# Kernel optimization log

Hardware: AMD Instinct MI355X
Metric: run time of the kernel (lower is better)

Reference implementation:

```python
import jax, jax.numpy as jnp
import numpy as np

B, N, DIM = 2, 2048, 1024
HEADS, DIM_HEAD = 16, 64
SOFTCAP = 50.0
ROPE_THETA = 10000.0


def setup_inputs() -> dict:
    key = jax.random.key(0)
    k1, k2, k3 = jax.random.split(key, 3)
    x = jax.random.normal(k1, (B, N, DIM), jnp.float32)
    # structured modality positions: (type, offset, length), non-overlapping, in-bounds
    mods = np.zeros((B, 4, 3), np.int64)
    base_offsets = [200, 700, 1200, 1700]
    for b in range(B):
        for m, o in enumerate(base_offsets):
            mods[b, m] = (0, o + b * 16, 256)
    modalities = jnp.asarray(mods)
    gamma = jnp.zeros((DIM,), jnp.float32)           # RMSNorm gamma (init zeros, used as gamma+1)
    w_qkv = jax.random.normal(k2, (DIM, 3 * HEADS * DIM_HEAD), jnp.float32) * 0.02
    w_out = jax.random.normal(k3, (HEADS * DIM_HEAD, DIM), jnp.float32) * 0.02
    return {"x": x, "modalities": modalities, "gamma": gamma, "w_qkv": w_qkv, "w_out": w_out}


def _rotate_half(x):
    # interleaved-pair rotation, matching rotary-embedding-torch default
    x1, x2 = x[..., 0::2], x[..., 1::2]
    return jnp.stack((-x2, x1), axis=-1).reshape(x.shape)


def reference(x, modalities, gamma, w_qkv, w_out):
    b, n, d = x.shape
    h, dh = HEADS, DIM_HEAD
    seq = jnp.arange(n)
    off = modalities[..., 1]      # [b, m]
    length = modalities[..., 2]   # [b, m]

    # --- modality-aware rotary positions (span interior shrunk by offset [1, -1]) ---
    in_span = (seq[None, None, :] >= (off + 1)[:, :, None]) & (seq[None, None, :] < (off + length)[:, :, None])
    is_any_modality = in_span.any(axis=1)                                   # [b, n]
    pos = (seq[None, :] - jnp.cumsum(is_any_modality.astype(jnp.int32), axis=-1)).astype(jnp.float32)

    # --- RMSNorm: l2norm(x) * sqrt(d) * (gamma + 1) ---
    norm = jnp.maximum(jnp.sqrt(jnp.sum(x * x, axis=-1, keepdims=True)), 1e-12)
    xn = x / norm * jnp.sqrt(jnp.float32(d)) * (gamma + 1.0)

    # --- qkv projection, split heads -> [b, h, n, dh] ---
    qkv = (xn @ w_qkv).reshape(b, n, 3, h, dh)
    q, k, v = jnp.moveaxis(qkv, 2, 0)        # each [b, n, h, dh]
    q = jnp.transpose(q, (0, 2, 1, 3))
    k = jnp.transpose(k, (0, 2, 1, 3))
    v = jnp.transpose(v, (0, 2, 1, 3))

    # --- rotary embedding with modality-aware positions ---
    inv_freq = ROPE_THETA ** (-jnp.arange(0, dh, 2, dtype=jnp.float32) / dh)  # [dh/2]
    ang = pos[:, None, :, None] * inv_freq                                    # [b, 1, n, dh/2]
    ang = jnp.repeat(ang, 2, axis=-1)                                         # [b, 1, n, dh]
    cos, sin = jnp.cos(ang), jnp.sin(ang)
    q = q * cos + _rotate_half(q) * sin
    k = k * cos + _rotate_half(k) * sin

    # --- transfusion attention mask: causal OR per-modality bidirectional span ---
    causal_mask = seq[:, None] >= seq[None, :]                                 # [n, n]
    q_ge = seq[None, None, :] >= off[:, :, None]                               # [b, m, n]
    kv_lt = seq[None, None, :] < (off + length)[:, :, None]                    # [b, m, n]
    mod_mask = (q_ge[:, :, :, None] & kv_lt[:, :, None, :]).any(axis=1)        # [b, n, n]
    mask = causal_mask[None] | mod_mask                                        # [b, n, n]

    # --- attention with softclamp(50) ---
    scale = dh ** -0.5
    sim = jnp.einsum('bhid,bhjd->bhij', q, k) * scale
    sim = jnp.tanh(sim / SOFTCAP) * SOFTCAP
    sim = jnp.where(mask[:, None], sim, jnp.finfo(sim.dtype).min)
    attn = jax.nn.softmax(sim, axis=-1)
    out = jnp.einsum('bhij,bhjd->bhid', attn, v)                               # [b, h, n, dh]
    out = jnp.transpose(out, (0, 2, 1, 3)).reshape(b, n, h * dh)
    return out @ w_out
```

## Files before the change

### kernel.cpp

```cpp
#include <hip/hip_runtime.h>
#include <hip/hip_bf16.h>
#include <stdint.h>

#define B_ 2
#define N_ 2048
#define H_ 16
#define DIM_ 1024
#define NH3 3072
#define ROWS (B_*N_)
#define BHN (B_*H_*N_)

typedef __attribute__((ext_vector_type(8))) short bf16x8;
typedef __attribute__((ext_vector_type(4))) float f32x4;
typedef unsigned short u16;

__device__ __forceinline__ u16 f2bf(float f){
  union { float f; uint32_t u; } v; v.f = f;
  return (u16)((v.u + 0x7fffu + ((v.u >> 16) & 1u)) >> 16);
}

#if __has_builtin(__builtin_amdgcn_exp2f)
#define EXP2F(x) __builtin_amdgcn_exp2f(x)
#else
#define EXP2F(x) __expf((x) * 0.6931471805599453f)
#endif
#if __has_builtin(__builtin_amdgcn_rcpf)
#define RCPF(x) __builtin_amdgcn_rcpf(x)
#else
#define RCPF(x) (1.0f / (x))
#endif

#define GLL16(g, l) __builtin_amdgcn_global_load_lds( \
    (const __attribute__((address_space(1))) void*)(g), \
    (__attribute__((address_space(3))) void*)(l), 16, 0, 0)

__global__ __launch_bounds__(256) void k_prep(
    const float* __restrict__ x, const float* __restrict__ gamma,
    const float* __restrict__ wqkv, const float* __restrict__ wout,
    const int* __restrict__ mods,
    u16* __restrict__ xn, u16* __restrict__ wqkvT, u16* __restrict__ woutT,
    float* __restrict__ cosT, float* __restrict__ sinT)
{
  __shared__ float tile[32][33];
  const int bx = blockIdx.x;
  const int tid = threadIdx.x;
  if (bx < 4096){
    const int row = bx;
    const float4 xv = ((const float4*)(x + (size_t)row*DIM_))[tid];
    float ss = xv.x*xv.x + xv.y*xv.y + xv.z*xv.z + xv.w*xv.w;
#pragma unroll
    for (int d = 1; d < 64; d <<= 1) ss += __shfl_xor(ss, d);
    if ((tid & 63) == 0) tile[1][tid >> 6] = ss;
    __syncthreads();
    float tot = tile[1][0] + tile[1][1] + tile[1][2] + tile[1][3];
    float scl = 32.0f / fmaxf(sqrtf(tot), 1e-12f);
    const float4 gv = ((const float4*)gamma)[tid];
    ushort4 o;
    o.x = f2bf(xv.x * scl * (gv.x + 1.0f));
    o.y = f2bf(xv.y * scl * (gv.y + 1.0f));
    o.z = f2bf(xv.z * scl * (gv.z + 1.0f));
    o.w = f2bf(xv.w * scl * (gv.w + 1.0f));
    ((ushort4*)(xn + (size_t)row*DIM_))[tid] = o;
  } else if (bx < 8192){
    const int t = bx - 4096;
    const int bxx = t & 127, by = t >> 7;
    const float* src; u16* dst; int C, bc;
    if (bxx < 96){ src = wqkv; dst = wqkvT; C = NH3;  bc = bxx*32; }
    else         { src = wout; dst = woutT; C = DIM_; bc = (bxx-96)*32; }
    const int R = DIM_;
    const int tx = tid & 31, ty = tid >> 5;
    const int br = by * 32;
#pragma unroll
    for (int i = 0; i < 32; i += 8)
      tile[ty + i][tx] = src[(size_t)(br + ty + i)*C + bc + tx];
    __syncthreads();
#pragma unroll
    for (int i = 0; i < 32; i += 8)
      dst[(size_t)(bc + ty + i)*R + br + tx] = f2bf(tile[tx][ty + i]);
  } else {
    const int t = (bx - 8192)*256 + tid;
    const int f = t & 31, bn = t >> 5;
    const int b = bn >> 11, n = bn & (N_-1);
    int cum = 0;
#pragma unroll
    for (int m = 0; m < 4; ++m){
      const int off = mods[(b*4 + m)*3 + 1];
      const int len = mods[(b*4 + m)*3 + 2];
      cum += min(max(n - off, 0), len - 1);
    }
    const float pos = (float)(n - cum);
    const float inv = powf(10000.0f, -(float)(2*f) / 64.0f);
    float s, c;
    sincosf(pos * inv, &s, &c);
    cosT[t] = c; sinT[t] = s;
  }
}

template<int MODE, int BM>
__global__ __launch_bounds__(256) void k_gemm(
    const u16* __restrict__ A, const u16* __restrict__ Bt,
    int K, int Nc,
    float* __restrict__ outf,
    const float* __restrict__ cosT, const float* __restrict__ sinT,
    u16* __restrict__ qo, u16* __restrict__ ko, u16* __restrict__ vt)
{
  constexpr int MR = BM/32;
  constexpr int RA = BM/8;
  constexpr int CNT = (RA + 16)/4;
  __shared__ u16 lA[BM*64];
  __shared__ u16 lB[128*64];
  const int tid = threadIdx.x;
  const int wid = tid >> 6, lane = tid & 63;
  const int nx = gridDim.x;
  const int orig = blockIdx.y * nx + blockIdx.x;
  const int qq = (nx * gridDim.y) >> 3;
  const int wgid = (orig & 7) * qq + (orig >> 3);
  const int m0 = (wgid % nx) * BM, n0 = (wgid / nx) * 128;
  const int wm = wid >> 1, wn = wid & 1;
  const int srow = lane >> 3, sch = lane & 7;
  const int r16 = lane & 15, g4 = lane >> 4;
  f32x4 acc[MR][4] = {};
  const int ksteps = K >> 6;
  for (int kt = 0; kt < ksteps; ++kt){
    const int kb = kt*64;
    const int gch = sch ^ srow;
#pragma unroll
    for (int i = 0; i < CNT; ++i){
      const int reg = wid*CNT + i;
      if (reg < RA){
        const int row = reg*8 + srow;
        GLL16(A + (size_t)(m0 + row)*K + kb + gch*8, &lA[reg*512]);
      } else {
        const int r2 = reg - RA;
        const int row = r2*8 + srow;
        GLL16(Bt + (size_t)(n0 + row)*K + kb + gch*8, &lB[r2*512]);
      }
    }
    __syncthreads();
#pragma unroll
    for (int t = 0; t < 2; ++t){
      bf16x8 af[MR], bfr[4];
#pragma unroll
      for (int m = 0; m < MR; ++m){
        int row = wm*(BM/2) + m*16 + r16;
        int ch = (t*4 + g4) ^ (r16 & 7);
        af[m] = *(const bf16x8*)&lA[row*64 + ch*8];
      }
#pragma unroll
      for (int n = 0; n < 4; ++n){
        int row = wn*64 + n*16 + r16;
        int ch = (t*4 + g4) ^ (r16 & 7);
        bfr[n] = *(const bf16x8*)&lB[row*64 + ch*8];
      }
#pragma unroll
      for (int m = 0; m < MR; ++m)
#pragma unroll
        for (int n = 0; n < 4; ++n)
          acc[m][n] = __builtin_amdgcn_mfma_f32_16x16x32_bf16(af[m], bfr[n], acc[m][n], 0, 0, 0);
    }
    __syncthreads();
  }
#pragma unroll
  for (int m = 0; m < MR; ++m){
#pragma unroll
    for (int n = 0; n < 4; ++n){
      if constexpr (MODE == 0){
        const int gcol = n0 + wn*64 + n*16 + r16;
        const int s3 = gcol >> 10, hh = (gcol >> 6) & 15, d = gcol & 63;
        const int grow0 = m0 + wm*(BM/2) + m*16 + g4*4;
        const int b = grow0 >> 11, nn0 = grow0 & (N_-1);
        const size_t hb = (size_t)(b*H_ + hh);
        if (s3 == 2){
          uint32_t w01, w23;
          asm("v_cvt_pk_bf16_f32 %0, %1, %2" : "=v"(w01) : "v"(acc[m][n][0]), "v"(acc[m][n][1]));
          asm("v_cvt_pk_bf16_f32 %0, %1, %2" : "=v"(w23) : "v"(acc[m][n][2]), "v"(acc[m][n][3]));
          *reinterpret_cast<uint2*>(&vt[(hb*64 + d)*N_ + nn0]) = make_uint2(w01, w23);
        } else {
#pragma unroll
          for (int r = 0; r < 4; ++r){
            const float v = acc[m][n][r];
            const float part = __shfl_xor(v, 1);
            const int nn = nn0 + r;
            const int pidx = (b*N_ + nn)*32 + (d >> 1);
            const float c = cosT[pidx], sn = sinT[pidx];
            const float rot = (d & 1) ? (v*c + part*sn) : (v*c - part*sn);
            const u16 val = f2bf(rot);
            if (s3 == 0) qo[(hb*N_ + nn)*64 + d] = val;
            else         ko[(hb*N_ + nn)*64 + d] = val;
          }
        }
      } else {
#pragma unroll
        for (int r = 0; r < 4; ++r){
          const int grow = m0 + wm*(BM/2) + m*16 + g4*4 + r;
          const int gcol = n0 + wn*64 + n*16 + r16;
          outf[(size_t)grow*Nc + gcol] = acc[m][n][r];
        }
      }
    }
  }
}

#define PST 68
__global__ __launch_bounds__(256) void k_attn(
    const u16* __restrict__ qb, const u16* __restrict__ kb, const u16* __restrict__ vt,
    const int* __restrict__ mods, u16* __restrict__ xo)
{
  __shared__ u16 lK[64*64];
  __shared__ u16 lV[64*64];
  __shared__ u16 lP[4*16*PST];
  const int tid = threadIdx.x, wid = tid >> 6, lane = tid & 63;
  const int id = blockIdx.x;
  const int xcd = id & 7, rank = id >> 3;
  const int bh = xcd + 8*(rank & 3);
  const int qt = 31 - (rank >> 2);
  const int b = bh >> 4, h = bh & 15;
  const int r16 = lane & 15, g4 = lane >> 4;
  const int srow = lane >> 3, sch = lane & 7;
  int moff[4], mend[4];
#pragma unroll
  for (int m = 0; m < 4; ++m){
    moff[m] = mods[(b*4+m)*3+1];
    mend[m] = moff[m] + mods[(b*4+m)*3+2];
  }
  const u16* kbase = kb + (size_t)bh*N_*64;
  const u16* vbase = vt + (size_t)bh*64*N_;
  u16* lPw = &lP[wid*16*PST];

  const int q0 = qt*64 + wid*16;
  const int i  = q0 + r16;
  const int imax = qt*64 + 63;
  int jmax = 0;
#pragma unroll
  for (int m = 0; m < 4; ++m)
    if (i >= moff[m]) jmax = max(jmax, mend[m]);
  const u16* qrow = qb + ((size_t)bh*N_ + q0 + r16)*64;
  const bf16x8 aq0 = *(const bf16x8*)&qrow[g4*8];
  const bf16x8 aq1 = *(const bf16x8*)&qrow[32 + g4*8];
  f32x4 o[4] = {};
  f32x4 acc_s = {};
  bf16x8 ones;
#pragma unroll
  for (int j = 0; j < 8; ++j) ones[j] = (short)0x3F80;

  const float D1 = 0.18033688011112043f;
  const float D3 = -3.7570183356483704e-07f;

  for (int kt = 0; kt < N_/64; ++kt){
    bool proc = (kt*64 <= imax);
    if (!proc){
#pragma unroll
      for (int m = 0; m < 4; ++m)
        if (imax >= moff[m] && kt*64 < mend[m]) proc = true;
    }
    if (!proc) continue;
    __syncthreads();
#pragma unroll
    for (int ld = 0; ld < 2; ++ld){
      int reg = wid*2 + ld;
      int row = reg*8 + srow;
      int gch = sch ^ srow;
      GLL16(kbase + (size_t)(kt*64 + row)*64 + gch*8, &lK[reg*512]);
      GLL16(vbase + (size_t)row*N_ + kt*64 + gch*8,   &lV[reg*512]);
    }
    __syncthreads();
    f32x4 s[4] = {};
    __builtin_amdgcn_s_setprio(1);
#pragma unroll
    for (int cb = 0; cb < 4; ++cb){
#pragma unroll
      for (int t = 0; t < 2; ++t){
        int row = cb*16 + r16;
        int ch = (t*4 + g4) ^ (row & 7);
        bf16x8 bk = *(const bf16x8*)&lK[row*64 + ch*8];
        s[cb] = __builtin_amdgcn_mfma_f32_16x16x32_bf16(bk, t ? aq1 : aq0, s[cb], 0, 0, 0);
      }
    }
    __builtin_amdgcn_s_setprio(0);
    const int thr = max(i, jmax - 1) - kt*64;
    const bool nomask = (kt*64 + 63 <= q0);
#pragma unroll
    for (int cb = 0; cb < 4; ++cb){
      float p[4];
#pragma unroll
      for (int r = 0; r < 4; ++r){
        const float sv = s[cb][r];
        const float w = sv*sv;
        p[r] = EXP2F(sv * fmaf(w, D3, D1));
      }
      if (!nomask){
#pragma unroll
        for (int r = 0; r < 4; ++r)
          p[r] = (cb*16 + g4*4 + r <= thr) ? p[r] : 0.0f;
      }
      uint32_t w01, w23;
      asm("v_cvt_pk_bf16_f32 %0, %1, %2" : "=v"(w01) : "v"(p[0]), "v"(p[1]));
      asm("v_cvt_pk_bf16_f32 %0, %1, %2" : "=v"(w23) : "v"(p[2]), "v"(p[3]));
      *reinterpret_cast<uint2*>(&lPw[r16*PST + cb*16 + g4*4]) = make_uint2(w01, w23);
    }
    asm volatile("s_waitcnt lgkmcnt(0)" ::: "memory");
    __builtin_amdgcn_sched_barrier(0);
    union { uint2 h[2]; bf16x8 v; } u0, u1;
    u0.h[0] = *(const uint2*)&lPw[r16*PST + g4*8];
    u0.h[1] = *(const uint2*)&lPw[r16*PST + g4*8 + 4];
    u1.h[0] = *(const uint2*)&lPw[r16*PST + 32 + g4*8];
    u1.h[1] = *(const uint2*)&lPw[r16*PST + 32 + g4*8 + 4];
    __builtin_amdgcn_s_setprio(1);
    acc_s = __builtin_amdgcn_mfma_f32_16x16x32_bf16(u0.v, ones, acc_s, 0, 0, 0);
    acc_s = __builtin_amdgcn_mfma_f32_16x16x32_bf16(u1.v, ones, acc_s, 0, 0, 0);
#pragma unroll
    for (int cb = 0; cb < 4; ++cb){
#pragma unroll
      for (int t = 0; t < 2; ++t){
        int d = cb*16 + r16;
        int ch = (t*4 + g4) ^ (d & 7);
        bf16x8 bv = *(const bf16x8*)&lV[d*64 + ch*8];
        o[cb] = __builtin_amdgcn_mfma_f32_16x16x32_bf16(t ? u1.v : u0.v, bv, o[cb], 0, 0, 0);
      }
    }
    __builtin_amdgcn_s_setprio(0);
  }
#pragma unroll
  for (int r = 0; r < 4; ++r){
    const float linv = RCPF(acc_s[r]);
    const int iq = q0 + g4*4 + r;
#pragma unroll
    for (int cb = 0; cb < 4; ++cb)
      xo[(size_t)(b*N_ + iq)*DIM_ + h*64 + cb*16 + r16] = f2bf(o[cb][r]*linv);
  }
}

extern "C" void kernel_launch(void* const* d_in, const int* in_sizes, int n_in,
                              void* d_out, int out_size, void* d_ws, size_t ws_size,
                              hipStream_t stream){
  const float* x     = (const float*)d_in[0];
  const int*   mods  = (const int*)d_in[1];
  const float* gamma = (const float*)d_in[2];
  const float* wqkv  = (const float*)d_in[3];
  const float* wout  = (const float*)d_in[4];
  float* outp = (float*)d_out;

  char* p = (char*)d_ws;
  auto alloc = [&](size_t bytes) -> char* {
    char* r = p; p += (bytes + 255) & ~(size_t)255; return r;
  };
  float* cosT  = (float*)alloc((size_t)B_*N_*32*4);
  float* sinT  = (float*)alloc((size_t)B_*N_*32*4);
  u16* wqkvT   = (u16*)alloc((size_t)NH3*DIM_*2);
  u16* woutT   = (u16*)alloc((size_t)DIM_*DIM_*2);
  u16* xn      = (u16*)alloc((size_t)ROWS*DIM_*2);
  u16* qbb     = (u16*)alloc((size_t)BHN*64*2);
  u16* kbb     = (u16*)alloc((size_t)BHN*64*2);
  u16* vtb     = (u16*)alloc((size_t)BHN*64*2);
  u16* xo      = (u16*)alloc((size_t)ROWS*DIM_*2);

  k_prep<<<8704, 256, 0, stream>>>(x, gamma, wqkv, wout, mods, xn, wqkvT, woutT, cosT, sinT);
  k_gemm<0,128><<<dim3(ROWS/128, NH3/128), 256, 0, stream>>>(xn, wqkvT, DIM_, NH3, nullptr, cosT, sinT, qbb, kbb, vtb);
  k_attn<<<1024, 256, 0, stream>>>(qbb, kbb, vtb, mods, xo);
  k_gemm<1,64><<<dim3(ROWS/64, DIM_/128), 256, 0, stream>>>(xo, woutT, DIM_, DIM_, outp, nullptr, nullptr, nullptr, nullptr, nullptr);
}
```

Before: 117.0 us.

## Process 128-key tiles per barrier pair with swizzled P layout and hoisted load addresses

Result: no change. 116.9 us (-0.2%).

```diff
diff --git a/kernel.cpp b/kernel.cpp
--- a/kernel.cpp
+++ b/kernel.cpp
@@ -201,14 +201,13 @@
   }
 }
 
-#define PST 68
 __global__ __launch_bounds__(256) void k_attn(
     const u16* __restrict__ qb, const u16* __restrict__ kb, const u16* __restrict__ vt,
     const int* __restrict__ mods, u16* __restrict__ xo)
 {
-  __shared__ u16 lK[64*64];
-  __shared__ u16 lV[64*64];
-  __shared__ u16 lP[4*16*PST];
+  __shared__ u16 lK[128*64];
+  __shared__ u16 lV[64*128];
+  __shared__ u16 lP[4*16*64];
   const int tid = threadIdx.x, wid = tid >> 6, lane = tid & 63;
   const int id = blockIdx.x;
   const int xcd = id & 7, rank = id >> 3;
@@ -216,7 +215,6 @@
   const int qt = 31 - (rank >> 2);
   const int b = bh >> 4, h = bh & 15;
   const int r16 = lane & 15, g4 = lane >> 4;
-  const int srow = lane >> 3, sch = lane & 7;
   int moff[4], mend[4];
 #pragma unroll
   for (int m = 0; m < 4; ++m){
@@ -225,7 +223,7 @@
   }
   const u16* kbase = kb + (size_t)bh*N_*64;
   const u16* vbase = vt + (size_t)bh*64*N_;
-  u16* lPw = &lP[wid*16*PST];
+  u16* lPw = &lP[wid*16*64];
 
   const int q0 = qt*64 + wid*16;
   const int i  = q0 + r16;
@@ -234,6 +232,7 @@
 #pragma unroll
   for (int m = 0; m < 4; ++m)
     if (i >= moff[m]) jmax = max(jmax, mend[m]);
+  const int thrbase = max(i, jmax - 1);
   const u16* qrow = qb + ((size_t)bh*N_ + q0 + r16)*64;
   const bf16x8 aq0 = *(const bf16x8*)&qrow[g4*8];
   const bf16x8 aq1 = *(const bf16x8*)&qrow[32 + g4*8];
@@ -243,82 +242,114 @@
 #pragma unroll
   for (int j = 0; j < 8; ++j) ones[j] = (short)0x3F80;
 
+  const int srow8 = lane >> 3, sch8 = lane & 7;
+  const int srow4 = lane >> 4, sch16 = lane & 15;
+  const u16* kSrc0; const u16* kSrc1; const u16* kSrc2; const u16* kSrc3;
+  const u16* vSrc0; const u16* vSrc1; const u16* vSrc2; const u16* vSrc3;
+  {
+    const int kch = sch8 ^ srow8;
+    kSrc0 = kbase + (size_t)((wid*4+0)*8 + srow8)*64 + kch*8;
+    kSrc1 = kbase + (size_t)((wid*4+1)*8 + srow8)*64 + kch*8;
+    kSrc2 = kbase + (size_t)((wid*4+2)*8 + srow8)*64 + kch*8;
+    kSrc3 = kbase + (size_t)((wid*4+3)*8 + srow8)*64 + kch*8;
+    const int d0 = (wid*4+0)*4 + srow4, d1 = (wid*4+1)*4 + srow4;
+    const int d2 = (wid*4+2)*4 + srow4, d3 = (wid*4+3)*4 + srow4;
+    vSrc0 = vbase + (size_t)d0*N_ + (sch16 ^ (d0 & 7))*8;
+    vSrc1 = vbase + (size_t)d1*N_ + (sch16 ^ (d1 & 7))*8;
+    vSrc2 = vbase + (size_t)d2*N_ + (sch16 ^ (d2 & 7))*8;
+    vSrc3 = vbase + (size_t)d3*N_ + (sch16 ^ (d3 & 7))*8;
+  }
+  const int pwr = r16*64 + (((g4 >> 1)) ^ (r16 & 7))*8 + (g4 & 1)*4;
   const float D1 = 0.18033688011112043f;
   const float D3 = -3.7570183356483704e-07f;
 
-  for (int kt = 0; kt < N_/64; ++kt){
-    bool proc = (kt*64 <= imax);
+  for (int kt = 0; kt < N_/128; ++kt){
+    const int kB = kt*128;
+    bool proc = (kB <= imax);
     if (!proc){
 #pragma unroll
       for (int m = 0; m < 4; ++m)
-        if (imax >= moff[m] && kt*64 < mend[m]) proc = true;
+        if (imax >= moff[m] && kB < mend[m]) proc = true;
     }
     if (!proc) continue;
-    __syncthreads();
-#pragma unroll
-    for (int ld = 0; ld < 2; ++ld){
-      int reg = wid*2 + ld;
-      int row = reg*8 + srow;
-      int gch = sch ^ srow;
-      GLL16(kbase + (size_t)(kt*64 + row)*64 + gch*8, &lK[reg*512]);
-      GLL16(vbase + (size_t)row*N_ + kt*64 + gch*8,   &lV[reg*512]);
-    }
-    __syncthreads();
-    f32x4 s[4] = {};
-    __builtin_amdgcn_s_setprio(1);
-#pragma unroll
-    for (int cb = 0; cb < 4; ++cb){
-#pragma unroll
-      for (int t = 0; t < 2; ++t){
-        int row = cb*16 + r16;
-        int ch = (t*4 + g4) ^ (row & 7);
-        bf16x8 bk = *(const bf16x8*)&lK[row*64 + ch*8];
-        s[cb] = __builtin_amdgcn_mfma_f32_16x16x32_bf16(bk, t ? aq1 : aq0, s[cb], 0, 0, 0);
-      }
-    }
-    __builtin_amdgcn_s_setprio(0);
-    const int thr = max(i, jmax - 1) - kt*64;
-    const bool nomask = (kt*64 + 63 <= q0);
-#pragma unroll
-    for (int cb = 0; cb < 4; ++cb){
-      float p[4];
-#pragma unroll
-      for (int r = 0; r < 4; ++r){
-        const float sv = s[cb][r];
-        const float w = sv*sv;
-        p[r] = EXP2F(sv * fmaf(w, D3, D1));
-      }
-      if (!nomask){
-#pragma unroll
-        for (int r = 0; r < 4; ++r)
-          p[r] = (cb*16 + g4*4 + r <= thr) ? p[r] : 0.0f;
-      }
-      uint32_t w01, w23;
-      asm("v_cvt_pk_bf16_f32 %0, %1, %2" : "=v"(w01) : "v"(p[0]), "v"(p[1]));
-      asm("v_cvt_pk_bf16_f32 %0, %1, %2" : "=v"(w23) : "v"(p[2]), "v"(p[3]));
-      *reinterpret_cast<uint2*>(&lPw[r16*PST + cb*16 + g4*4]) = make_uint2(w01, w23);
-    }
-    asm volatile("s_waitcnt lgkmcnt(0)" ::: "memory");
-    __builtin_amdgcn_sched_barrier(0);
-    union { uint2 h[2]; bf16x8 v; } u0, u1;
-    u0.h[0] = *(const uint2*)&lPw[r16*PST + g4*8];
-    u0.h[1] = *(const uint2*)&lPw[r16*PST + g4*8 + 4];
-    u1.h[0] = *(const uint2*)&lPw[r16*PST + 32 + g4*8];
-    u1.h[1] = *(const uint2*)&lPw[r16*PST + 32 + g4*8 + 4];
-    __builtin_amdgcn_s_setprio(1);
-    acc_s = __builtin_amdgcn_mfma_f32_16x16x32_bf16(u0.v, ones, acc_s, 0, 0, 0);
-    acc_s = __builtin_amdgcn_mfma_f32_16x16x32_bf16(u1.v, ones, acc_s, 0, 0, 0);
-#pragma unroll
-    for (int cb = 0; cb < 4; ++cb){
-#pragma unroll
-      for (int t = 0; t < 2; ++t){
-        int d = cb*16 + r16;
-        int ch = (t*4 + g4) ^ (d & 7);
-        bf16x8 bv = *(const bf16x8*)&lV[d*64 + ch*8];
-        o[cb] = __builtin_amdgcn_mfma_f32_16x16x32_bf16(t ? u1.v : u0.v, bv, o[cb], 0, 0, 0);
-      }
-    }
-    __builtin_amdgcn_s_setprio(0);
+    bool proc1 = (kB + 64 <= imax);
+    if (!proc1){
+#pragma unroll
+      for (int m = 0; m < 4; ++m)
+        if (imax >= moff[m] && kB + 64 < mend[m]) proc1 = true;
+    }
+    __syncthreads();
+    {
+      const size_t kOff = (size_t)kB*64;
+      GLL16(kSrc0 + kOff, &lK[(wid*4+0)*512]);
+      GLL16(kSrc1 + kOff, &lK[(wid*4+1)*512]);
+      GLL16(kSrc2 + kOff, &lK[(wid*4+2)*512]);
+      GLL16(kSrc3 + kOff, &lK[(wid*4+3)*512]);
+      GLL16(vSrc0 + kB, &lV[(wid*4+0)*512]);
+      GLL16(vSrc1 + kB, &lV[(wid*4+1)*512]);
+      GLL16(vSrc2 + kB, &lV[(wid*4+2)*512]);
+      GLL16(vSrc3 + kB, &lV[(wid*4+3)*512]);
+    }
+    __syncthreads();
+
+#pragma unroll
+    for (int hh2 = 0; hh2 < 2; ++hh2){
+      if (hh2 == 1 && !proc1) break;
+      f32x4 s[4] = {};
+      __builtin_amdgcn_s_setprio(1);
+#pragma unroll
+      for (int cb = 0; cb < 4; ++cb){
+#pragma unroll
+        for (int t = 0; t < 2; ++t){
+          int row = hh2*64 + cb*16 + r16;
+          int ch = (t*4 + g4) ^ (r16 & 7);
+          bf16x8 bk = *(const bf16x8*)&lK[row*64 + ch*8];
+          s[cb] = __builtin_amdgcn_mfma_f32_16x16x32_bf16(bk, t ? aq1 : aq0, s[cb], 0, 0, 0);
+        }
+      }
+      __builtin_amdgcn_s_setprio(0);
+      const int kb64 = kB + hh2*64;
+      const int thr = thrbase - kb64;
+      const bool nomask = (kb64 + 63 <= q0);
+#pragma unroll
+      for (int cb = 0; cb < 4; ++cb){
+        float p[4];
+#pragma unroll
+        for (int r = 0; r < 4; ++r){
+          const float sv = s[cb][r];
+          const float w = sv*sv;
+          p[r] = EXP2F(sv * fmaf(w, D3, D1));
+        }
+        if (!nomask){
+#pragma unroll
+          for (int r = 0; r < 4; ++r)
+            p[r] = (cb*16 + g4*4 + r <= thr) ? p[r] : 0.0f;
+        }
+        uint32_t w01, w23;
+        asm("v_cvt_pk_bf16_f32 %0, %1, %2" : "=v"(w01) : "v"(p[0]), "v"(p[1]));
+        asm("v_cvt_pk_bf16_f32 %0, %1, %2" : "=v"(w23) : "v"(p[2]), "v"(p[3]));
+        const int pos = (cb*2 + (g4 >> 1)) ^ (r16 & 7);
+        *reinterpret_cast<uint2*>(&lPw[r16*64 + pos*8 + (g4 & 1)*4]) = make_uint2(w01, w23);
+      }
+      asm volatile("s_waitcnt lgkmcnt(0)" ::: "memory");
+      __builtin_amdgcn_sched_barrier(0);
+      const bf16x8 ap0 = *(const bf16x8*)&lPw[r16*64 + ((g4)     ^ (r16 & 7))*8];
+      const bf16x8 ap1 = *(const bf16x8*)&lPw[r16*64 + ((4 + g4) ^ (r16 & 7))*8];
+      __builtin_amdgcn_s_setprio(1);
+      acc_s = __builtin_amdgcn_mfma_f32_16x16x32_bf16(ap0, ones, acc_s, 0, 0, 0);
+      acc_s = __builtin_amdgcn_mfma_f32_16x16x32_bf16(ap1, ones, acc_s, 0, 0, 0);
+#pragma unroll
+      for (int cb = 0; cb < 4; ++cb){
+#pragma unroll
+        for (int t = 0; t < 2; ++t){
+          int d = cb*16 + r16;
+          int ch = (hh2*8 + t*4 + g4) ^ (r16 & 7);
+          bf16x8 bv = *(const bf16x8*)&lV[d*128 + ch*8];
+          o[cb] = __builtin_amdgcn_mfma_f32_16x16x32_bf16(t ? ap1 : ap0, bv, o[cb], 0, 0, 0);
+        }
+      }
+      __builtin_amdgcn_s_setprio(0);
+    }
   }
 #pragma unroll
   for (int r = 0; r < 4; ++r){
@@ -328,6 +359,7 @@
     for (int cb = 0; cb < 4; ++cb)
       xo[(size_t)(b*N_ + iq)*DIM_ + h*64 + cb*16 + r16] = f2bf(o[cb][r]*linv);
   }
+  (void)pwr;
 }
 
 extern "C" void kernel_launch(void* const* d_in, const int* in_sizes, int n_in,
```
